# Performance work log

Hardware: AMD Instinct MI355X
Metric: run time of the kernel (lower is better)

## Reference

```python
import jax, jax.numpy as jnp
import numpy as np

NL = 4      # num_hidden_layers
NH = 12     # self-attn heads
CH = 4      # cross-attn heads (hardcoded in module)
S = 4       # speakers per dialog
EPS = 1e-5

def layernorm(x, g, b):
    m = x.mean(-1, keepdims=True)
    v = jnp.mean((x - m) ** 2, axis=-1, keepdims=True)
    return (x - m) * jax.lax.rsqrt(v + EPS) * g + b

def self_mha(x, in_w, in_b, out_w, out_b):
    # x: [B,T,L,H] self-attention over L (the per-turn token axis)
    B, T, L, H = x.shape
    dh = H // NH
    qkv = x @ in_w + in_b                       # [B,T,L,3H]
    q, k, v = jnp.split(qkv, 3, axis=-1)
    q = q.reshape(B, T, L, NH, dh); k = k.reshape(B, T, L, NH, dh); v = v.reshape(B, T, L, NH, dh)
    s = jnp.einsum('btqhd,btkhd->bthqk', q, k) / np.sqrt(dh).astype(x.dtype)
    a = jax.nn.softmax(s, axis=-1)
    o = jnp.einsum('bthqk,btkhd->btqhd', a, v).reshape(B, T, L, H)
    return o @ out_w + out_b

def forward(input_ids, attention_mask, speaker_ids, tok_emb, pos_emb, turn_emb,
            mha_in_w, mha_in_b, mha_out_w, mha_out_b,
            ffn_w1, ffn_b1, ffn_w2, ffn_b2,
            ln1_g, ln1_b, ln2_g, ln2_b,
            gate_w, gate_b, sn_g, sn_b,
            ca_in_w, ca_in_b, ca_out_w, ca_out_b):
    B, T, L = input_ids.shape
    H = tok_emb.shape[1]
    X = tok_emb[input_ids] + pos_emb[jnp.arange(L)][None, None] + turn_emb[jnp.arange(T)][None, :, None]
    mask = attention_mask[..., None].astype(X.dtype)            # [B,T,L,1]
    onehot = (speaker_ids[..., None] == jnp.arange(S)).astype(X.dtype)  # [B,T,S]
    counts = onehot.sum(1)                                      # [B,S]
    M = jnp.zeros((B, S, H), X.dtype)                           # speaker memory
    for l in range(NL):
        m_t = jnp.einsum('bts,bsh->bth', onehot, M)             # gather memory per turn
        h = (X + m_t[:, :, None, :]) * mask                     # mask applied by zeroing inputs (as in source)
        h = self_mha(h, mha_in_w[l], mha_in_b[l], mha_out_w[l], mha_out_b[l])
        h = layernorm(h + X, ln1_g[l], ln1_b[l])
        ffn = jax.nn.gelu(h @ ffn_w1[l] + ffn_b1[l], approximate=False) @ ffn_w2[l] + ffn_b2[l]
        h = layernorm(h + ffn, ln2_g[l], ln2_b[l])
        X = h
        tc = h.mean(2)                                          # token_context [B,T,H]
        # cross-attention: each turn's context queries its dialog's speaker memory
        wq, wk, wv = jnp.split(ca_in_w[l], 3, axis=-1)
        bq, bk, bv = jnp.split(ca_in_b[l], 3)
        dh = H // CH
        q = (tc @ wq + bq).reshape(B, T, CH, dh)
        k = (M @ wk + bk).reshape(B, S, CH, dh)
        v = (M @ wv + bv).reshape(B, S, CH, dh)
        s = jnp.einsum('bthd,bshd->bhts', q, k) / np.sqrt(dh).astype(X.dtype)
        a = jax.nn.softmax(s, axis=-1)
        cc = jnp.einsum('bhts,bshd->bthd', a, v).reshape(B, T, H) @ ca_out_w[l] + ca_out_b[l]
        fused = jnp.concatenate([tc, m_t, cc], axis=-1)         # [B,T,3H]
        upd = layernorm(fused @ gate_w[l] + gate_b[l] + m_t, sn_g[l], sn_b[l])
        # scatter: per-speaker mean over that speaker's turns; untouched speakers keep old memory
        sums = jnp.einsum('bts,bth->bsh', onehot, upd)
        mean = sums / jnp.maximum(counts, 1.0)[..., None]
        M = jnp.where((counts > 0)[..., None], mean, M)
    return X, M

def setup_inputs() -> dict:
    key = jax.random.key(0)
    ks = iter(jax.random.split(key, 32))
    B, T, L, H, F, V, P = 8, 64, 64, 768, 3072, 30522, 512
    n = lambda shape: jax.random.normal(next(ks), shape, jnp.float32) * 0.02
    return {
        'input_ids': jax.random.randint(next(ks), (B, T, L), 0, V, jnp.int32),
        'attention_mask': jax.random.randint(next(ks), (B, T, L), 0, 2, jnp.int32),
        'speaker_ids': jax.random.randint(next(ks), (B, T), 0, S, jnp.int32),
        'tok_emb': n((V, H)), 'pos_emb': n((P, H)), 'turn_emb': n((P, H)),
        'mha_in_w': n((NL, H, 3 * H)), 'mha_in_b': jnp.zeros((NL, 3 * H)),
        'mha_out_w': n((NL, H, H)), 'mha_out_b': jnp.zeros((NL, H)),
        'ffn_w1': n((NL, H, F)), 'ffn_b1': jnp.zeros((NL, F)),
        'ffn_w2': n((NL, F, H)), 'ffn_b2': jnp.zeros((NL, H)),
        'ln1_g': jnp.ones((NL, H)), 'ln1_b': jnp.zeros((NL, H)),
        'ln2_g': jnp.ones((NL, H)), 'ln2_b': jnp.zeros((NL, H)),
        'gate_w': n((NL, 3 * H, H)), 'gate_b': jnp.zeros((NL, H)),
        'sn_g': jnp.ones((NL, H)), 'sn_b': jnp.zeros((NL, H)),
        'ca_in_w': n((NL, H, 3 * H)), 'ca_in_b': jnp.zeros((NL, 3 * H)),
        'ca_out_w': n((NL, H, H)), 'ca_out_b': jnp.zeros((NL, H)),
    }

def reference(input_ids, attention_mask, speaker_ids, tok_emb, pos_emb, turn_emb,
              mha_in_w, mha_in_b, mha_out_w, mha_out_b,
              ffn_w1, ffn_b1, ffn_w2, ffn_b2,
              ln1_g, ln1_b, ln2_g, ln2_b,
              gate_w, gate_b, sn_g, sn_b,
              ca_in_w, ca_in_b, ca_out_w, ca_out_b):
    return forward(input_ids, attention_mask, speaker_ids, tok_emb, pos_emb, turn_emb,
                   mha_in_w, mha_in_b, mha_out_w, mha_out_b,
                   ffn_w1, ffn_b1, ffn_w2, ffn_b2,
                   ln1_g, ln1_b, ln2_g, ln2_b,
                   gate_w, gate_b, sn_g, sn_b,
                   ca_in_w, ca_in_b, ca_out_w, ca_out_b)
```

## Files before the change

### kernel.cpp

```cpp
#include <hip/hip_runtime.h>

using u16 = unsigned short;
using u32 = unsigned int;

#define DI __device__ __forceinline__

typedef __bf16 bf16x8 __attribute__((ext_vector_type(8)));
typedef float  f32x4  __attribute__((ext_vector_type(4)));

DI float b2f(u16 u){ u32 x = ((u32)u) << 16; float f; __builtin_memcpy(&f, &x, 4); return f; }
DI u16 f2b(float f){ __bf16 h = (__bf16)f; u16 r; __builtin_memcpy(&r, &h, 2); return r; }
DI float gelu_fast(float v){
    float u = v * (0.7978845608f + 0.0356774081f * v * v);
    float e = __expf(2.0f * u);
    float t = 1.0f - 2.0f / (e + 1.0f);
    return 0.5f * v * (1.0f + t);
}

#define GLOAD16(g, l) __builtin_amdgcn_global_load_lds( \
    (const __attribute__((address_space(1))) void*)(g), \
    (__attribute__((address_space(3))) void*)(l), 16, 0, 0)

DI bf16x8 ldsr128(const u16* p) {
    bf16x8 r;
    asm volatile("ds_read_b128 %0, %1"
                 : "=v"(r)
                 : "v"((const __attribute__((address_space(3))) u16*)p));
    return r;
}

template<int EPI>
__global__ __launch_bounds__(512, 1)
void gemm256p(const u16* __restrict__ A, const u16* __restrict__ Bt,
              const float* __restrict__ bias, void* __restrict__ Cout,
              int M, int N, int K)
{
    __shared__ u16 lA[2][256 * 64];
    __shared__ u16 lB[2][256 * 64];
    const int tid  = threadIdx.x;
    const int lane = tid & 63;
    const int w    = tid >> 6;
    const int wm   = w >> 2, wn = w & 3;

    const int nx = gridDim.x;
    const int nb = nx * gridDim.y;
    int bid = blockIdx.y * nx + blockIdx.x;
    if ((nb & 7) == 0) bid = ((bid & 7) * (nb >> 3)) + (bid >> 3);
    const int m0 = (bid / nx) * 256;
    const int n0 = (bid % nx) * 256;

    f32x4 acc[8][4] = {};

    const int srowb = w * 32 + (lane >> 3);
    const int csrc  = ((lane & 7) ^ ((lane >> 3) & 7)) * 8;
    const u16* gA[4];
    const u16* gB[4];
    #pragma unroll
    for (int i = 0; i < 4; ++i) {
        int ra = m0 + srowb + i * 8; if (ra > M - 1) ra = M - 1;
        gA[i] = A  + (size_t)ra * K + csrc;
        gB[i] = Bt + (size_t)(n0 + srowb + i * 8) * K + csrc;
    }

    const int la = lane & 15, lg = lane >> 4;
    const int nt = K >> 6;

    #pragma unroll
    for (int i = 0; i < 4; ++i) GLOAD16(gA[i], &lA[0][(w * 256 + i * 64 + lane) * 8]);
    #pragma unroll
    for (int i = 0; i < 4; ++i) GLOAD16(gB[i], &lB[0][(w * 256 + i * 64 + lane) * 8]);
    asm volatile("s_waitcnt vmcnt(0)" ::: "memory");
    __builtin_amdgcn_s_barrier();
    asm volatile("" ::: "memory");

    for (int t = 0; t < nt; ++t) {
        const int p = t & 1;
        const u16* lAp = lA[p];
        const u16* lBp = lB[p];
        u16* dA = lA[p ^ 1];
        u16* dB = lB[p ^ 1];
        const int kn = (t + 1) << 6;
        const bool more = (t + 1 < nt);

        bf16x8 bf[4][2];

        #pragma unroll
        for (int ph = 0; ph < 4; ++ph) {
            if (ph == 0) {
                #pragma unroll
                for (int j = 0; j < 4; ++j) {
                    bf[j][0] = ldsr128(&lBp[(wn * 64 + j * 16 + la) * 64 + (((0 * 4 + lg) ^ (la & 7)) * 8)]);
                    bf[j][1] = ldsr128(&lBp[(wn * 64 + j * 16 + la) * 64 + (((1 * 4 + lg) ^ (la & 7)) * 8)]);
                }
            }
            bf16x8 a0k0 = ldsr128(&lAp[(wm * 128 + (2 * ph) * 16 + la) * 64     + (((0 * 4 + lg) ^ (la & 7)) * 8)]);
            bf16x8 a0k1 = ldsr128(&lAp[(wm * 128 + (2 * ph) * 16 + la) * 64     + (((1 * 4 + lg) ^ (la & 7)) * 8)]);
            bf16x8 a1k0 = ldsr128(&lAp[(wm * 128 + (2 * ph + 1) * 16 + la) * 64 + (((0 * 4 + lg) ^ (la & 7)) * 8)]);
            bf16x8 a1k1 = ldsr128(&lAp[(wm * 128 + (2 * ph + 1) * 16 + la) * 64 + (((1 * 4 + lg) ^ (la & 7)) * 8)]);

            if (ph == 0 && more) {
                #pragma unroll
                for (int i = 0; i < 4; ++i) GLOAD16(gA[i] + kn, &dA[(w * 256 + i * 64 + lane) * 8]);
            }
            if (ph == 1 && more) {
                #pragma unroll
                for (int i = 0; i < 4; ++i) GLOAD16(gB[i] + kn, &dB[(w * 256 + i * 64 + lane) * 8]);
            }

            __builtin_amdgcn_s_barrier();
            asm volatile("s_waitcnt lgkmcnt(0)" ::: "memory");
            __builtin_amdgcn_sched_barrier(0);

            __builtin_amdgcn_s_setprio(1);
            #pragma unroll
            for (int j = 0; j < 4; ++j) {
                acc[2 * ph][j]     = __builtin_amdgcn_mfma_f32_16x16x32_bf16(a0k0, bf[j][0], acc[2 * ph][j],     0, 0, 0);
                acc[2 * ph + 1][j] = __builtin_amdgcn_mfma_f32_16x16x32_bf16(a1k0, bf[j][0], acc[2 * ph + 1][j], 0, 0, 0);
            }
            #pragma unroll
            for (int j = 0; j < 4; ++j) {
                acc[2 * ph][j]     = __builtin_amdgcn_mfma_f32_16x16x32_bf16(a0k1, bf[j][1], acc[2 * ph][j],     0, 0, 0);
                acc[2 * ph + 1][j] = __builtin_amdgcn_mfma_f32_16x16x32_bf16(a1k1, bf[j][1], acc[2 * ph + 1][j], 0, 0, 0);
            }
            __builtin_amdgcn_s_setprio(0);

            if (ph == 3) {
                asm volatile("s_waitcnt vmcnt(0)" ::: "memory");
            }
            __builtin_amdgcn_s_barrier();
            asm volatile("" ::: "memory");
        }
    }

    #pragma unroll
    for (int i = 0; i < 8; i++) {
        const int rowb = m0 + wm * 128 + i * 16 + lg * 4;
        #pragma unroll
        for (int j = 0; j < 4; j++) {
            const int col = n0 + wn * 64 + j * 16 + la;
            const float bv = bias[col];
            #pragma unroll
            for (int r = 0; r < 4; r++) {
                const int rr = rowb + r;
                if (rr < M) {
                    float v = acc[i][j][r] + bv;
                    if constexpr (EPI == 1) v = gelu_fast(v);
                    if constexpr (EPI == 2) ((float*)Cout)[(size_t)rr * N + col] = v;
                    else                    ((u16*)Cout)[(size_t)rr * N + col] = f2b(v);
                }
            }
        }
    }
}

template<int EPI>
__global__ __launch_bounds__(256)
void gemm_bt(const u16* __restrict__ A, const u16* __restrict__ Bt,
             const float* __restrict__ bias, void* __restrict__ Cout,
             int M, int N, int K)
{
    __shared__ u16 lA[3][128 * 32];
    __shared__ u16 lB[3][128 * 32];
    const int tid  = threadIdx.x;
    const int lane = tid & 63;
    const int w    = tid >> 6;
    const int wm   = w >> 1, wn = w & 1;

    const int nx = gridDim.x;
    const int nb = nx * gridDim.y;
    int bid = blockIdx.y * nx + blockIdx.x;
    if ((nb & 7) == 0) bid = ((bid & 7) * (nb >> 3)) + (bid >> 3);
    const int m0 = (bid / nx) * 128;
    const int n0 = (bid % nx) * 128;

    f32x4 acc[4][4] = {};

    const int srow = tid >> 2;
    const int scol = (((tid & 3) ^ ((tid >> 3) & 3)) * 8);
    int ar0 = m0 + srow;      if (ar0 > M - 1) ar0 = M - 1;
    int ar1 = m0 + 64 + srow; if (ar1 > M - 1) ar1 = M - 1;
    const u16* gA0 = A  + (size_t)ar0 * K + scol;
    const u16* gA1 = A  + (size_t)ar1 * K + scol;
    const u16* gB0 = Bt + (size_t)(n0 + srow) * K + scol;
    const u16* gB1 = Bt + (size_t)(n0 + 64 + srow) * K + scol;

    const int la = lane & 15, lg = lane >> 4;
    const int cp = (lg ^ ((la >> 1) & 3)) * 8;

    const int nt = K >> 5;

    GLOAD16(gA0,      &lA[0][tid * 8]);
    GLOAD16(gA1,      &lA[0][tid * 8 + 2048]);
    GLOAD16(gB0,      &lB[0][tid * 8]);
    GLOAD16(gB1,      &lB[0][tid * 8 + 2048]);
    GLOAD16(gA0 + 32, &lA[1][tid * 8]);
    GLOAD16(gA1 + 32, &lA[1][tid * 8 + 2048]);
    GLOAD16(gB0 + 32, &lB[1][tid * 8]);
    GLOAD16(gB1 + 32, &lB[1][tid * 8 + 2048]);

    int cur = 0, pre = 2;
    for (int t = 0; t < nt; ++t) {
        if (t + 1 < nt) asm volatile("s_waitcnt vmcnt(4)" ::: "memory");
        else            asm volatile("s_waitcnt vmcnt(0)" ::: "memory");
        __builtin_amdgcn_s_barrier();
        asm volatile("" ::: "memory");

        if (t + 2 < nt) {
            const int k0 = (t + 2) << 5;
            GLOAD16(gA0 + k0, &lA[pre][tid * 8]);
            GLOAD16(gA1 + k0, &lA[pre][tid * 8 + 2048]);
            GLOAD16(gB0 + k0, &lB[pre][tid * 8]);
            GLOAD16(gB1 + k0, &lB[pre][tid * 8 + 2048]);
        }

        bf16x8 af[4], bfr[4];
        #pragma unroll
        for (int i = 0; i < 4; i++)
            af[i] = ldsr128(&lA[cur][(wm * 64 + i * 16 + la) * 32 + cp]);
        #pragma unroll
        for (int j = 0; j < 4; j++)
            bfr[j] = ldsr128(&lB[cur][(wn * 64 + j * 16 + la) * 32 + cp]);
        asm volatile("s_waitcnt lgkmcnt(0)" ::: "memory");
        __builtin_amdgcn_sched_barrier(0);

        #pragma unroll
        for (int i = 0; i < 4; i++)
            #pragma unroll
            for (int j = 0; j < 4; j++)
                acc[i][j] = __builtin_amdgcn_mfma_f32_16x16x32_bf16(af[i], bfr[j], acc[i][j], 0, 0, 0);

        cur = (cur == 2) ? 0 : cur + 1;
        pre = (pre == 2) ? 0 : pre + 1;
    }

    #pragma unroll
    for (int i = 0; i < 4; i++) {
        const int rowb = m0 + wm * 64 + i * 16 + lg * 4;
        #pragma unroll
        for (int j = 0; j < 4; j++) {
            const int col = n0 + wn * 64 + j * 16 + la;
            const float bv = bias[col];
            #pragma unroll
            for (int r = 0; r < 4; r++) {
                const int rr = rowb + r;
                if (rr < M) {
                    float v = acc[i][j][r] + bv;
                    if constexpr (EPI == 1) v = gelu_fast(v);
                    if constexpr (EPI == 2) ((float*)Cout)[(size_t)rr * N + col] = v;
                    else                    ((u16*)Cout)[(size_t)rr * N + col] = f2b(v);
                }
            }
        }
    }
}

__global__ __launch_bounds__(256)
void transp_conv(const float* __restrict__ in, u16* __restrict__ out, int K, int N)
{
    __shared__ float tile[32][33];
    const int l = blockIdx.z;
    const float* inp = in + (size_t)l * K * N;
    u16* op = out + (size_t)l * K * N;
    const int kb = blockIdx.y * 32, nb = blockIdx.x * 32;
    const int tx = threadIdx.x, ty = threadIdx.y;
    #pragma unroll
    for (int i = 0; i < 32; i += 8)
        tile[ty + i][tx] = inp[(size_t)(kb + ty + i) * N + nb + tx];
    __syncthreads();
    #pragma unroll
    for (int i = 0; i < 32; i += 8)
        op[(size_t)(nb + ty + i) * K + kb + tx] = f2b(tile[tx][ty + i]);
}

__global__ __launch_bounds__(192)
void embed_k(const int* __restrict__ ids, const float* __restrict__ te,
             const float* __restrict__ pe, const float* __restrict__ ue,
             u16* __restrict__ X)
{
    const int tok = blockIdx.x;
    const int l = tok & 63;
    const int t = (tok >> 6) & 63;
    const int id = ids[tok];
    const int c = threadIdx.x * 4;
    float4 a = *(const float4*)&te[(size_t)id * 768 + c];
    float4 p = *(const float4*)&pe[(size_t)l * 768 + c];
    float4 u = *(const float4*)&ue[(size_t)t * 768 + c];
    ushort4 o;
    o.x = f2b(a.x + p.x + u.x); o.y = f2b(a.y + p.y + u.y);
    o.z = f2b(a.z + p.z + u.z); o.w = f2b(a.w + p.w + u.w);
    *(ushort4*)&X[(size_t)tok * 768 + c] = o;
}

__global__ __launch_bounds__(192)
void gather_mt(const float* __restrict__ M, const int* __restrict__ sid,
               float* __restrict__ mt)
{
    const int bt = blockIdx.x, b = bt >> 6, tid = threadIdx.x;
    const float* src = M + ((size_t)b * 4 + sid[bt]) * 768;
    *(float4*)&mt[(size_t)bt * 768 + tid * 4] = *(const float4*)&src[tid * 4];
}

__global__ __launch_bounds__(192)
void prep_ain(const u16* __restrict__ X, const float* __restrict__ mt,
              const int* __restrict__ mask, u16* __restrict__ Ain)
{
    const int tok = blockIdx.x, bt = tok >> 6;
    const float mk = (float)mask[tok];
    const int c = threadIdx.x * 4;
    ushort4 xv = *(const ushort4*)&X[(size_t)tok * 768 + c];
    float4 mv = *(const float4*)&mt[(size_t)bt * 768 + c];
    ushort4 o;
    o.x = f2b((b2f(xv.x) + mv.x) * mk); o.y = f2b((b2f(xv.y) + mv.y) * mk);
    o.z = f2b((b2f(xv.z) + mv.z) * mk); o.w = f2b((b2f(xv.w) + mv.w) * mk);
    *(ushort4*)&Ain[(size_t)tok * 768 + c] = o;
}

DI int swz(int row, int col) { return row * 64 + (((col >> 3) ^ (row & 7)) << 3) + (col & 7); }

__global__ __launch_bounds__(256)
void attn_self(const u16* __restrict__ QKV, u16* __restrict__ O)
{
    __shared__ u16 lQ[64 * 64], lK[64 * 64], lVt[64 * 64], lP[64 * 64];
    __shared__ float lS[64 * 68];
    const int bt = blockIdx.x / 12, h = blockIdx.x % 12;
    const int tid = threadIdx.x, lane = tid & 63, w = tid >> 6;
    const size_t base = (size_t)bt * 64 * 2304;

    #pragma unroll
    for (int it = 0; it < 2; ++it) {
        const int slot = it * 256 + tid;
        const int l = slot >> 3, dc = (slot & 7) * 8;
        const u16* qp = QKV + base + (size_t)l * 2304 + h * 64 + dc;
        *(uint4*)&lQ[swz(l, dc)] = *(const uint4*)qp;
        *(uint4*)&lK[swz(l, dc)] = *(const uint4*)(qp + 768);
        uint4 vv = *(const uint4*)(qp + 1536);
        u16 tmp[8]; *(uint4*)tmp = vv;
        #pragma unroll
        for (int j = 0; j < 8; j++) lVt[swz(dc + j, l)] = tmp[j];
    }
    __syncthreads();

    const int la = lane & 15, lg = lane >> 4;
    {
        f32x4 sa[4] = {};
        #pragma unroll
        for (int kh = 0; kh < 64; kh += 32) {
            bf16x8 aq = *(const bf16x8*)&lQ[swz(w * 16 + la, kh + lg * 8)];
            #pragma unroll
            for (int fn = 0; fn < 4; ++fn) {
                bf16x8 bk = *(const bf16x8*)&lK[swz(fn * 16 + la, kh + lg * 8)];
                sa[fn] = __builtin_amdgcn_mfma_f32_16x16x32_bf16(aq, bk, sa[fn], 0, 0, 0);
            }
        }
        #pragma unroll
        for (int fn = 0; fn < 4; ++fn)
            #pragma unroll
            for (int r = 0; r < 4; ++r)
                lS[(w * 16 + lg * 4 + r) * 68 + fn * 16 + la] = sa[fn][r] * 0.125f;
    }
    __syncthreads();

    {
        const int row = tid >> 2, q4 = tid & 3;
        float e[16]; float mx = -1e30f;
        #pragma unroll
        for (int j = 0; j < 16; j++) { e[j] = lS[row * 68 + q4 * 16 + j]; mx = fmaxf(mx, e[j]); }
        mx = fmaxf(mx, __shfl_xor(mx, 1)); mx = fmaxf(mx, __shfl_xor(mx, 2));
        float sm = 0.f;
        #pragma unroll
        for (int j = 0; j < 16; j++) { e[j] = __expf(e[j] - mx); sm += e[j]; }
        sm += __shfl_xor(sm, 1); sm += __shfl_xor(sm, 2);
        const float inv = 1.0f / sm;
        #pragma unroll
        for (int j = 0; j < 16; j++) lP[swz(row, q4 * 16 + j)] = f2b(e[j] * inv);
    }
    __syncthreads();

    {
        f32x4 oa[4] = {};
        #pragma unroll
        for (int kh = 0; kh < 64; kh += 32) {
            bf16x8 ap = *(const bf16x8*)&lP[swz(w * 16 + la, kh + lg * 8)];
            #pragma unroll
            for (int fn = 0; fn < 4; ++fn) {
                bf16x8 bv = *(const bf16x8*)&lVt[swz(fn * 16 + la, kh + lg * 8)];
                oa[fn] = __builtin_amdgcn_mfma_f32_16x16x32_bf16(ap, bv, oa[fn], 0, 0, 0);
            }
        }
        const size_t ob = (size_t)bt * 64 * 768 + h * 64;
        #pragma unroll
        for (int fn = 0; fn < 4; ++fn)
            #pragma unroll
            for (int r = 0; r < 4; ++r)
                O[ob + (size_t)(w * 16 + lg * 4 + r) * 768 + fn * 16 + la] = f2b(oa[fn][r]);
    }
}

DI float wave_red(float v) {
    #pragma unroll
    for (int o = 32; o > 0; o >>= 1) v += __shfl_xor(v, o);
    return v;
}

__global__ __launch_bounds__(192)
void ln_res(const u16* __restrict__ a, const u16* __restrict__ b,
            const float* __restrict__ g, const float* __restrict__ be,
            u16* __restrict__ out)
{
    __shared__ float red[6];
    const int tid = threadIdx.x, w = tid >> 6;
    const size_t off = (size_t)blockIdx.x * 768 + tid * 4;
    ushort4 av = *(const ushort4*)&a[off];
    ushort4 bv = *(const ushort4*)&b[off];
    float x0 = b2f(av.x) + b2f(bv.x);
    float x1 = b2f(av.y) + b2f(bv.y);
    float x2 = b2f(av.z) + b2f(bv.z);
    float x3 = b2f(av.w) + b2f(bv.w);
    float s  = wave_red(x0 + x1 + x2 + x3);
    float ss = wave_red(x0 * x0 + x1 * x1 + x2 * x2 + x3 * x3);
    if ((tid & 63) == 0) { red[w] = s; red[3 + w] = ss; }
    __syncthreads();
    s = red[0] + red[1] + red[2];
    ss = red[3] + red[4] + red[5];
    const float mean = s * (1.f / 768.f);
    const float var = fmaxf(ss * (1.f / 768.f) - mean * mean, 0.f);
    const float inv = rsqrtf(var + 1e-5f);
    const int c = tid * 4;
    float4 gv = *(const float4*)&g[c];
    float4 ev = *(const float4*)&be[c];
    ushort4 o;
    o.x = f2b((x0 - mean) * inv * gv.x + ev.x);
    o.y = f2b((x1 - mean) * inv * gv.y + ev.y);
    o.z = f2b((x2 - mean) * inv * gv.z + ev.z);
    o.w = f2b((x3 - mean) * inv * gv.w + ev.w);
    *(ushort4*)&out[off] = o;
}

__global__ __launch_bounds__(192)
void ln_upd(const float* __restrict__ a, const float* __restrict__ b,
            const float* __restrict__ g, const float* __restrict__ be,
            float* __restrict__ out)
{
    __shared__ float red[6];
    const int tid = threadIdx.x, w = tid >> 6;
    const size_t off = (size_t)blockIdx.x * 768 + tid * 4;
    float4 av = *(const float4*)&a[off];
    float4 bv = *(const float4*)&b[off];
    float x0 = av.x + bv.x, x1 = av.y + bv.y, x2 = av.z + bv.z, x3 = av.w + bv.w;
    float s  = wave_red(x0 + x1 + x2 + x3);
    float ss = wave_red(x0 * x0 + x1 * x1 + x2 * x2 + x3 * x3);
    if ((tid & 63) == 0) { red[w] = s; red[3 + w] = ss; }
    __syncthreads();
    s = red[0] + red[1] + red[2];
    ss = red[3] + red[4] + red[5];
    const float mean = s * (1.f / 768.f);
    const float var = fmaxf(ss * (1.f / 768.f) - mean * mean, 0.f);
    const float inv = rsqrtf(var + 1e-5f);
    const int c = tid * 4;
    float4 gv = *(const float4*)&g[c];
    float4 ev = *(const float4*)&be[c];
    float4 o;
    o.x = (x0 - mean) * inv * gv.x + ev.x;
    o.y = (x1 - mean) * inv * gv.y + ev.y;
    o.z = (x2 - mean) * inv * gv.z + ev.z;
    o.w = (x3 - mean) * inv * gv.w + ev.w;
    *(float4*)&out[off] = o;
}

__global__ __launch_bounds__(192)
void tc_mean(const u16* __restrict__ X, u16* __restrict__ tcb)
{
    const int bt = blockIdx.x, tid = threadIdx.x;
    const u16* base = X + (size_t)bt * 64 * 768 + tid * 4;
    float s0 = 0, s1 = 0, s2 = 0, s3 = 0;
    for (int l = 0; l < 64; ++l) {
        ushort4 v = *(const ushort4*)&base[(size_t)l * 768];
        s0 += b2f(v.x); s1 += b2f(v.y); s2 += b2f(v.z); s3 += b2f(v.w);
    }
    ushort4 o;
    o.x = f2b(s0 * (1.f / 64.f)); o.y = f2b(s1 * (1.f / 64.f));
    o.z = f2b(s2 * (1.f / 64.f)); o.w = f2b(s3 * (1.f / 64.f));
    *(ushort4*)&tcb[(size_t)bt * 768 + tid * 4] = o;
}

__global__ __launch_bounds__(256)
void conv_bf16(const float* __restrict__ in, u16* __restrict__ out, int n)
{
    const int i = blockIdx.x * 256 + threadIdx.x;
    if (i < n) out[i] = f2b(in[i]);
}

__global__ __launch_bounds__(256)
void zero_f32(float* __restrict__ buf, int n)
{
    const int i = blockIdx.x * 256 + threadIdx.x;
    if (i < n) buf[i] = 0.f;
}

__global__ __launch_bounds__(256)
void cross_attn(const u16* __restrict__ qc, const u16* __restrict__ kvc,
                u16* __restrict__ cca)
{
    __shared__ float q[768], kk[4][768], vv[4][768], sraw[16], aw[16];
    const int bt = blockIdx.x, b = bt >> 6, tid = threadIdx.x;
    #pragma unroll
    for (int i = 0; i < 3; i++) q[tid + i * 256] = b2f(qc[(size_t)bt * 768 + tid + i * 256]);
    #pragma unroll
    for (int i = 0; i < 12; i++) {
        const int idx = i * 256 + tid;
        const int s = idx / 768, d = idx % 768;
        kk[s][d] = b2f(kvc[(size_t)(b * 4 + s) * 1536 + d]);
        vv[s][d] = b2f(kvc[(size_t)(b * 4 + s) * 1536 + 768 + d]);
    }
    __syncthreads();
    if (tid < 16) {
        const int hh = tid >> 2, s = tid & 3;
        float acc = 0.f;
        for (int d = 0; d < 192; ++d) acc += q[hh * 192 + d] * kk[s][hh * 192 + d];
        sraw[tid] = acc * 0.07216878364870323f;
    }
    __syncthreads();
    if (tid < 4) {
        float m = -1e30f;
        for (int s = 0; s < 4; s++) m = fmaxf(m, sraw[tid * 4 + s]);
        float ee[4], sm = 0.f;
        for (int s = 0; s < 4; s++) { ee[s] = __expf(sraw[tid * 4 + s] - m); sm += ee[s]; }
        for (int s = 0; s < 4; s++) aw[tid * 4 + s] = ee[s] / sm;
    }
    __syncthreads();
    #pragma unroll
    for (int i = 0; i < 3; i++) {
        const int j = tid + i * 256;
        const int hh = j / 192;
        float v = aw[hh * 4 + 0] * vv[0][j] + aw[hh * 4 + 1] * vv[1][j]
                + aw[hh * 4 + 2] * vv[2][j] + aw[hh * 4 + 3] * vv[3][j];
        cca[(size_t)bt * 768 + j] = f2b(v);
    }
}

__global__ __launch_bounds__(256)
void concat_fused(const u16* __restrict__ tcb, const float* __restrict__ mt,
                  const u16* __restrict__ ccp, u16* __restrict__ Fu)
{
    const int bt = blockIdx.x, tid = threadIdx.x;
    u16* o = Fu + (size_t)bt * 2304;
    #pragma unroll
    for (int i = 0; i < 3; i++) {
        const int j = tid + i * 256;
        o[j]        = tcb[(size_t)bt * 768 + j];
        o[768 + j]  = f2b(mt[(size_t)bt * 768 + j]);
        o[1536 + j] = ccp[(size_t)bt * 768 + j];
    }
}

__global__ __launch_bounds__(256)
void scatter_mem(const float* __restrict__ upd, const int* __restrict__ sid,
                 const float* __restrict__ counts, float* __restrict__ M)
{
    const int bs = blockIdx.x, b = bs >> 2, s = bs & 3, tid = threadIdx.x;
    const float c = counts[bs];
    #pragma unroll
    for (int i = 0; i < 3; i++) {
        const int j = tid + i * 256;
        float acc = 0.f;
        for (int t = 0; t < 64; ++t)
            if (sid[b * 64 + t] == s) acc += upd[((size_t)b * 64 + t) * 768 + j];
        if (c > 0.f) M[(size_t)bs * 768 + j] = acc / fmaxf(c, 1.f);
    }
}

__global__ void calc_counts(const int* __restrict__ sid, float* __restrict__ counts)
{
    const int tid = threadIdx.x;
    if (tid < 32) {
        const int b = tid >> 2, s = tid & 3;
        float c = 0.f;
        for (int t = 0; t < 64; ++t) c += (sid[b * 64 + t] == s) ? 1.f : 0.f;
        counts[tid] = c;
    }
}

__global__ __launch_bounds__(256)
void final_out(const u16* __restrict__ Xb, const float* __restrict__ M,
               float* __restrict__ out)
{
    const size_t i4 = ((size_t)blockIdx.x * 256 + threadIdx.x) * 4;
    const size_t NX = 25165824ull;
    if (i4 < NX) {
        ushort4 v = *(const ushort4*)&Xb[i4];
        float4 o; o.x = b2f(v.x); o.y = b2f(v.y); o.z = b2f(v.z); o.w = b2f(v.w);
        *(float4*)&out[i4] = o;
    } else if (i4 < NX + 24576ull) {
        *(float4*)&out[i4] = *(const float4*)&M[i4 - NX];
    }
}

extern "C" void kernel_launch(void* const* d_in, const int* in_sizes, int n_in,
                              void* d_out, int out_size, void* d_ws, size_t ws_size,
                              hipStream_t stream)
{
    const int*   input_ids = (const int*)d_in[0];
    const int*   attn_mask = (const int*)d_in[1];
    const int*   sid       = (const int*)d_in[2];
    const float* tok_emb   = (const float*)d_in[3];
    const float* pos_emb   = (const float*)d_in[4];
    const float* turn_emb  = (const float*)d_in[5];
    const float* mha_in_w  = (const float*)d_in[6];
    const float* mha_in_b  = (const float*)d_in[7];
    const float* mha_out_w = (const float*)d_in[8];
    const float* mha_out_b = (const float*)d_in[9];
    const float* ffn_w1    = (const float*)d_in[10];
    const float* ffn_b1    = (const float*)d_in[11];
    const float* ffn_w2    = (const float*)d_in[12];
    const float* ffn_b2    = (const float*)d_in[13];
    const float* ln1_g     = (const float*)d_in[14];
    const float* ln1_b     = (const float*)d_in[15];
    const float* ln2_g     = (const float*)d_in[16];
    const float* ln2_b     = (const float*)d_in[17];
    const float* gate_w    = (const float*)d_in[18];
    const float* gate_b    = (const float*)d_in[19];
    const float* sn_g      = (const float*)d_in[20];
    const float* sn_b      = (const float*)d_in[21];
    const float* ca_in_w   = (const float*)d_in[22];
    const float* ca_in_b   = (const float*)d_in[23];
    const float* ca_out_w  = (const float*)d_in[24];
    const float* ca_out_b  = (const float*)d_in[25];
    (void)in_sizes; (void)n_in; (void)out_size;

    const size_t MB = 1ull << 20;
    int NCA, NCF; bool allW;
    if      (ws_size >= 460 * MB) { NCA = 2; NCF = 1; allW = true;  }
    else if (ws_size >= 340 * MB) { NCA = 2; NCF = 2; allW = true;  }
    else if (ws_size >= 255 * MB) { NCA = 2; NCF = 2; allW = false; }
    else                          { NCA = 4; NCF = 4; allW = false; }
    const int MRA = 32768 / NCA;
    const int MRF = 32768 / NCF;
    const size_t wl = allW ? 4 : 1;

    char* p = (char*)d_ws;
    auto alloc = [&](size_t n) { void* r = p; p += (n + 255) & ~(size_t)255; return r; };
    u16*   Xb    = (u16*)alloc(50331648);
    u16*   Hb    = (u16*)alloc(50331648);
    u16*   WqkvT = (u16*)alloc(wl * 3538944);
    u16*   WoT   = (u16*)alloc(wl * 1179648);
    u16*   W1T   = (u16*)alloc(wl * 4718592);
    u16*   W2T   = (u16*)alloc(wl * 4718592);
    u16*   WgT   = (u16*)alloc(wl * 3538944);
    u16*   WcaT  = (u16*)alloc(wl * 3538944);
    u16*   WcoT  = (u16*)alloc(wl * 1179648);
    float* mt    = (float*)alloc(1572864);
    u16*   tcb   = (u16*)alloc(786432);
    u16*   Mb    = (u16*)alloc(49152);
    u16*   qc    = (u16*)alloc(786432);
    u16*   kvc   = (u16*)alloc(98304);
    u16*   cca   = (u16*)alloc(786432);
    u16*   ccp   = (u16*)alloc(786432);
    u16*   Fu    = (u16*)alloc(2359296);
    float* gout  = (float*)alloc(1572864);
    float* upd   = (float*)alloc(1572864);
    float* cnts  = (float*)alloc(256);
    float* M     = (float*)alloc(98304);

    u16 *A, *QKVb, *Gb;
    if (NCF == 1) {
        A    = (u16*)alloc(50331648);
        Gb   = (u16*)alloc(201326592);
        QKVb = (u16*)d_out;
    } else if (NCF == 2) {
        A    = (u16*)alloc(50331648);
        QKVb = (u16*)alloc((size_t)MRA * 2304 * 2);
        Gb   = (u16*)d_out;
    } else {
        Gb   = (u16*)alloc((size_t)MRF * 3072 * 2);
        A    = (u16*)d_out;
        QKVb = (u16*)d_out + 25165824;
    }
    u16* Obuf = Gb;

    zero_f32<<<96, 256, 0, stream>>>(M, 24576);
    calc_counts<<<1, 64, 0, stream>>>(sid, cnts);
    embed_k<<<32768, 192, 0, stream>>>(input_ids, tok_emb, pos_emb, turn_emb, Xb);

    if (allW) {
        transp_conv<<<dim3(72, 24, 4), dim3(32, 8), 0, stream>>>(mha_in_w,  WqkvT, 768, 2304);
        transp_conv<<<dim3(24, 24, 4), dim3(32, 8), 0, stream>>>(mha_out_w, WoT,   768, 768);
        transp_conv<<<dim3(96, 24, 4), dim3(32, 8), 0, stream>>>(ffn_w1,    W1T,   768, 3072);
        transp_conv<<<dim3(24, 96, 4), dim3(32, 8), 0, stream>>>(ffn_w2,    W2T,  3072, 768);
        transp_conv<<<dim3(24, 72, 4), dim3(32, 8), 0, stream>>>(gate_w,    WgT,  2304, 768);
        transp_conv<<<dim3(72, 24, 4), dim3(32, 8), 0, stream>>>(ca_in_w,   WcaT,  768, 2304);
        transp_conv<<<dim3(24, 24, 4), dim3(32, 8), 0, stream>>>(ca_out_w,  WcoT,  768, 768);
    }

    for (int l = 0; l < 4; ++l) {
        if (!allW) {
            transp_conv<<<dim3(72, 24), dim3(32, 8), 0, stream>>>(mha_in_w  + (size_t)l * 768 * 2304, WqkvT, 768, 2304);
            transp_conv<<<dim3(24, 24), dim3(32, 8), 0, stream>>>(mha_out_w + (size_t)l * 768 * 768,  WoT,   768, 768);
            transp_conv<<<dim3(96, 24), dim3(32, 8), 0, stream>>>(ffn_w1    + (size_t)l * 768 * 3072, W1T,   768, 3072);
            transp_conv<<<dim3(24, 96), dim3(32, 8), 0, stream>>>(ffn_w2    + (size_t)l * 3072 * 768, W2T,  3072, 768);
            transp_conv<<<dim3(24, 72), dim3(32, 8), 0, stream>>>(gate_w    + (size_t)l * 2304 * 768, WgT,  2304, 768);
            transp_conv<<<dim3(72, 24), dim3(32, 8), 0, stream>>>(ca_in_w   + (size_t)l * 768 * 2304, WcaT,  768, 2304);
            transp_conv<<<dim3(24, 24), dim3(32, 8), 0, stream>>>(ca_out_w  + (size_t)l * 768 * 768,  WcoT,  768, 768);
        }
        const u16* Wqkv_l = WqkvT + (size_t)(allW ? l : 0) * 2304 * 768;
        const u16* Wo_l   = WoT   + (size_t)(allW ? l : 0) * 768 * 768;
        const u16* W1_l   = W1T   + (size_t)(allW ? l : 0) * 768 * 3072;
        const u16* W2_l   = W2T   + (size_t)(allW ? l : 0) * 3072 * 768;
        const u16* Wg_l   = WgT   + (size_t)(allW ? l : 0) * 2304 * 768;
        const u16* Wca_l  = WcaT  + (size_t)(allW ? l : 0) * 768 * 2304;
        const u16* Wco_l  = WcoT  + (size_t)(allW ? l : 0) * 768 * 768;

        gather_mt<<<512, 192, 0, stream>>>(M, sid, mt);
        prep_ain<<<32768, 192, 0, stream>>>(Xb, mt, attn_mask, A);

        for (int c = 0; c < NCA; ++c) {
            u16* Ac = A + (size_t)c * MRA * 768;
            gemm256p<0><<<dim3(9, MRA / 256), 512, 0, stream>>>(Ac, Wqkv_l, mha_in_b + l * 2304, QKVb, MRA, 2304, 768);
            attn_self<<<(MRA / 64) * 12, 256, 0, stream>>>(QKVb, Obuf);
            gemm_bt<0><<<dim3(6, MRA / 128), 256, 0, stream>>>(Obuf, Wo_l, mha_out_b + l * 768, Ac, MRA, 768, 768);
        }
        ln_res<<<32768, 192, 0, stream>>>(A, Xb, ln1_g + l * 768, ln1_b + l * 768, Hb);

        for (int c = 0; c < NCF; ++c) {
            u16* Hc = Hb + (size_t)c * MRF * 768;
            u16* Ac = A  + (size_t)c * MRF * 768;
            gemm256p<1><<<dim3(12, MRF / 256), 512, 0, stream>>>(Hc, W1_l, ffn_b1 + l * 3072, Gb, MRF, 3072, 768);
            gemm_bt<0><<<dim3(6, MRF / 128), 256, 0, stream>>>(Gb, W2_l, ffn_b2 + l * 768, Ac, MRF, 768, 3072);
        }
        ln_res<<<32768, 192, 0, stream>>>(A, Hb, ln2_g + l * 768, ln2_b + l * 768, Xb);

        tc_mean<<<512, 192, 0, stream>>>(Xb, tcb);
        conv_bf16<<<96, 256, 0, stream>>>(M, Mb, 24576);
        gemm_bt<0><<<dim3(6, 4), 256, 0, stream>>>(tcb, Wca_l, ca_in_b + l * 2304, qc, 512, 768, 768);
        gemm_bt<0><<<dim3(12, 1), 256, 0, stream>>>(Mb, Wca_l + 768 * 768, ca_in_b + l * 2304 + 768, kvc, 32, 1536, 768);
        cross_attn<<<512, 256, 0, stream>>>(qc, kvc, cca);
        gemm_bt<0><<<dim3(6, 4), 256, 0, stream>>>(cca, Wco_l, ca_out_b + l * 768, ccp, 512, 768, 768);
        concat_fused<<<512, 256, 0, stream>>>(tcb, mt, ccp, Fu);
        gemm_bt<2><<<dim3(6, 4), 256, 0, stream>>>(Fu, Wg_l, gate_b + l * 768, gout, 512, 768, 2304);
        ln_upd<<<512, 192, 0, stream>>>(gout, mt, sn_g + l * 768, sn_b + l * 768, upd);
        scatter_mem<<<32, 256, 0, stream>>>(upd, sid, cnts, M);
    }

    final_out<<<24600, 256, 0, stream>>>(Xb, M, (float*)d_out);
}
```

Before: 4.186 ms.

## Switch 256x256 GEMM to triple-buffered K=32 pipeline with two-stage prefetch

The 256x256 MFMA GEMM used for the QKV and FFN-up projections now uses three LDS stages of K=32 in place of two stages of K=64. Global-to-LDS loads run two tiles ahead, with a new swizzle and load mapping for the narrower tile. This aims to hide global memory latency better while keeping the LDS footprint about the same. In exchange it halves the MFMA work per barrier and adds more barriers and waitcnt bookkeeping per K step.

```diff
diff --git a/kernel.cpp b/kernel.cpp
--- a/kernel.cpp
+++ b/kernel.cpp
@@ -31,12 +31,12 @@
 
 template<int EPI>
 __global__ __launch_bounds__(512, 1)
-void gemm256p(const u16* __restrict__ A, const u16* __restrict__ Bt,
+void gemm256c(const u16* __restrict__ A, const u16* __restrict__ Bt,
               const float* __restrict__ bias, void* __restrict__ Cout,
               int M, int N, int K)
 {
-    __shared__ u16 lA[2][256 * 64];
-    __shared__ u16 lB[2][256 * 64];
+    __shared__ u16 lA[3][256 * 32];
+    __shared__ u16 lB[3][256 * 32];
     const int tid  = threadIdx.x;
     const int lane = tid & 63;
     const int w    = tid >> 6;
@@ -51,85 +51,94 @@
 
     f32x4 acc[8][4] = {};
 
-    const int srowb = w * 32 + (lane >> 3);
-    const int csrc  = ((lane & 7) ^ ((lane >> 3) & 7)) * 8;
-    const u16* gA[4];
-    const u16* gB[4];
-    #pragma unroll
-    for (int i = 0; i < 4; ++i) {
-        int ra = m0 + srowb + i * 8; if (ra > M - 1) ra = M - 1;
-        gA[i] = A  + (size_t)ra * K + csrc;
-        gB[i] = Bt + (size_t)(n0 + srowb + i * 8) * K + csrc;
-    }
+    const int srow = tid >> 2;
+    const int scol = (((tid & 3) ^ ((tid >> 3) & 3)) * 8);
+    int ar0 = m0 + srow;       if (ar0 > M - 1) ar0 = M - 1;
+    int ar1 = m0 + 128 + srow; if (ar1 > M - 1) ar1 = M - 1;
+    const u16* gA0 = A  + (size_t)ar0 * K + scol;
+    const u16* gA1 = A  + (size_t)ar1 * K + scol;
+    const u16* gB0 = Bt + (size_t)(n0 + srow) * K + scol;
+    const u16* gB1 = Bt + (size_t)(n0 + 128 + srow) * K + scol;
 
     const int la = lane & 15, lg = lane >> 4;
-    const int nt = K >> 6;
-
-    #pragma unroll
-    for (int i = 0; i < 4; ++i) GLOAD16(gA[i], &lA[0][(w * 256 + i * 64 + lane) * 8]);
-    #pragma unroll
-    for (int i = 0; i < 4; ++i) GLOAD16(gB[i], &lB[0][(w * 256 + i * 64 + lane) * 8]);
-    asm volatile("s_waitcnt vmcnt(0)" ::: "memory");
+    const int cp = (lg ^ ((la >> 1) & 3)) * 8;
+
+    const int nt = K >> 5;
+
+    GLOAD16(gA0,      &lA[0][tid * 8]);
+    GLOAD16(gA1,      &lA[0][4096 + tid * 8]);
+    GLOAD16(gB0,      &lB[0][tid * 8]);
+    GLOAD16(gB1,      &lB[0][4096 + tid * 8]);
+    GLOAD16(gA0 + 32, &lA[1][tid * 8]);
+    GLOAD16(gA1 + 32, &lA[1][4096 + tid * 8]);
+    GLOAD16(gB0 + 32, &lB[1][tid * 8]);
+    GLOAD16(gB1 + 32, &lB[1][4096 + tid * 8]);
+
+    asm volatile("s_waitcnt vmcnt(4)" ::: "memory");
     __builtin_amdgcn_s_barrier();
     asm volatile("" ::: "memory");
 
+    int cur = 0;
     for (int t = 0; t < nt; ++t) {
-        const int p = t & 1;
-        const u16* lAp = lA[p];
-        const u16* lBp = lB[p];
-        u16* dA = lA[p ^ 1];
-        u16* dB = lB[p ^ 1];
-        const int kn = (t + 1) << 6;
-        const bool more = (t + 1 < nt);
-
-        bf16x8 bf[4][2];
-
-        #pragma unroll
-        for (int ph = 0; ph < 4; ++ph) {
-            if (ph == 0) {
-                #pragma unroll
-                for (int j = 0; j < 4; ++j) {
-                    bf[j][0] = ldsr128(&lBp[(wn * 64 + j * 16 + la) * 64 + (((0 * 4 + lg) ^ (la & 7)) * 8)]);
-                    bf[j][1] = ldsr128(&lBp[(wn * 64 + j * 16 + la) * 64 + (((1 * 4 + lg) ^ (la & 7)) * 8)]);
-                }
-            }
-            bf16x8 a0k0 = ldsr128(&lAp[(wm * 128 + (2 * ph) * 16 + la) * 64     + (((0 * 4 + lg) ^ (la & 7)) * 8)]);
-            bf16x8 a0k1 = ldsr128(&lAp[(wm * 128 + (2 * ph) * 16 + la) * 64     + (((1 * 4 + lg) ^ (la & 7)) * 8)]);
-            bf16x8 a1k0 = ldsr128(&lAp[(wm * 128 + (2 * ph + 1) * 16 + la) * 64 + (((0 * 4 + lg) ^ (la & 7)) * 8)]);
-            bf16x8 a1k1 = ldsr128(&lAp[(wm * 128 + (2 * ph + 1) * 16 + la) * 64 + (((1 * 4 + lg) ^ (la & 7)) * 8)]);
-
-            if (ph == 0 && more) {
-                #pragma unroll
-                for (int i = 0; i < 4; ++i) GLOAD16(gA[i] + kn, &dA[(w * 256 + i * 64 + lane) * 8]);
-            }
-            if (ph == 1 && more) {
-                #pragma unroll
-                for (int i = 0; i < 4; ++i) GLOAD16(gB[i] + kn, &dB[(w * 256 + i * 64 + lane) * 8]);
-            }
-
-            __builtin_amdgcn_s_barrier();
-            asm volatile("s_waitcnt lgkmcnt(0)" ::: "memory");
-            __builtin_amdgcn_sched_barrier(0);
-
-            __builtin_amdgcn_s_setprio(1);
-            #pragma unroll
-            for (int j = 0; j < 4; ++j) {
-                acc[2 * ph][j]     = __builtin_amdgcn_mfma_f32_16x16x32_bf16(a0k0, bf[j][0], acc[2 * ph][j],     0, 0, 0);
-                acc[2 * ph + 1][j] = __builtin_amdgcn_mfma_f32_16x16x32_bf16(a1k0, bf[j][0], acc[2 * ph + 1][j], 0, 0, 0);
-            }
-            #pragma unroll
-            for (int j = 0; j < 4; ++j) {
-                acc[2 * ph][j]     = __builtin_amdgcn_mfma_f32_16x16x32_bf16(a0k1, bf[j][1], acc[2 * ph][j],     0, 0, 0);
-                acc[2 * ph + 1][j] = __builtin_amdgcn_mfma_f32_16x16x32_bf16(a1k1, bf[j][1], acc[2 * ph + 1][j], 0, 0, 0);
-            }
-            __builtin_amdgcn_s_setprio(0);
-
-            if (ph == 3) {
-                asm volatile("s_waitcnt vmcnt(0)" ::: "memory");
-            }
-            __builtin_amdgcn_s_barrier();
-            asm volatile("" ::: "memory");
-        }
+        const u16* lAp = lA[cur];
+        const u16* lBp = lB[cur];
+        const int nxt = (cur >= 1) ? cur - 1 : cur + 2;
+        const int k2 = (t + 2) << 5;
+        const bool more = (t + 2 < nt);
+
+        bf16x8 bfr[4], af[4];
+
+        #pragma unroll
+        for (int j = 0; j < 4; ++j)
+            bfr[j] = ldsr128(&lBp[(wn * 64 + j * 16 + la) * 32 + cp]);
+        #pragma unroll
+        for (int i = 0; i < 4; ++i)
+            af[i] = ldsr128(&lAp[(wm * 128 + i * 16 + la) * 32 + cp]);
+        if (more) {
+            GLOAD16(gA0 + k2, &lA[nxt][tid * 8]);
+            GLOAD16(gA1 + k2, &lA[nxt][4096 + tid * 8]);
+        }
+        __builtin_amdgcn_s_barrier();
+        asm volatile("s_waitcnt lgkmcnt(0)" ::: "memory");
+        __builtin_amdgcn_sched_barrier(0);
+
+        __builtin_amdgcn_s_setprio(1);
+        #pragma unroll
+        for (int i = 0; i < 4; ++i)
+            #pragma unroll
+            for (int j = 0; j < 4; ++j)
+                acc[i][j] = __builtin_amdgcn_mfma_f32_16x16x32_bf16(af[i], bfr[j], acc[i][j], 0, 0, 0);
+        __builtin_amdgcn_s_setprio(0);
+        __builtin_amdgcn_s_barrier();
+        asm volatile("" ::: "memory");
+
+        #pragma unroll
+        for (int i = 0; i < 4; ++i)
+            af[i] = ldsr128(&lAp[(wm * 128 + (i + 4) * 16 + la) * 32 + cp]);
+        if (more) {
+            GLOAD16(gB0 + k2, &lB[nxt][tid * 8]);
+            GLOAD16(gB1 + k2, &lB[nxt][4096 + tid * 8]);
+        }
+        __builtin_amdgcn_s_barrier();
+        asm volatile("s_waitcnt lgkmcnt(0)" ::: "memory");
+        __builtin_amdgcn_sched_barrier(0);
+
+        __builtin_amdgcn_s_setprio(1);
+        #pragma unroll
+        for (int i = 0; i < 4; ++i)
+            #pragma unroll
+            for (int j = 0; j < 4; ++j)
+                acc[i + 4][j] = __builtin_amdgcn_mfma_f32_16x16x32_bf16(af[i], bfr[j], acc[i + 4][j], 0, 0, 0);
+        __builtin_amdgcn_s_setprio(0);
+
+        if (t + 1 < nt) {
+            if (more) asm volatile("s_waitcnt vmcnt(4)" ::: "memory");
+            else      asm volatile("s_waitcnt vmcnt(0)" ::: "memory");
+        }
+        __builtin_amdgcn_s_barrier();
+        asm volatile("" ::: "memory");
+
+        cur = (cur + 1 == 3) ? 0 : cur + 1;
     }
 
     #pragma unroll
@@ -714,7 +723,7 @@
 
         for (int c = 0; c < NCA; ++c) {
             u16* Ac = A + (size_t)c * MRA * 768;
-            gemm256p<0><<<dim3(9, MRA / 256), 512, 0, stream>>>(Ac, Wqkv_l, mha_in_b + l * 2304, QKVb, MRA, 2304, 768);
+            gemm256c<0><<<dim3(9, MRA / 256), 512, 0, stream>>>(Ac, Wqkv_l, mha_in_b + l * 2304, QKVb, MRA, 2304, 768);
             attn_self<<<(MRA / 64) * 12, 256, 0, stream>>>(QKVb, Obuf);
             gemm_bt<0><<<dim3(6, MRA / 128), 256, 0, stream>>>(Obuf, Wo_l, mha_out_b + l * 768, Ac, MRA, 768, 768);
         }
@@ -723,7 +732,7 @@
         for (int c = 0; c < NCF; ++c) {
             u16* Hc = Hb + (size_t)c * MRF * 768;
             u16* Ac = A  + (size_t)c * MRF * 768;
-            gemm256p<1><<<dim3(12, MRF / 256), 512, 0, stream>>>(Hc, W1_l, ffn_b1 + l * 3072, Gb, MRF, 3072, 768);
+            gemm256c<1><<<dim3(12, MRF / 256), 512, 0, stream>>>(Hc, W1_l, ffn_b1 + l * 3072, Gb, MRF, 3072, 768);
             gemm_bt<0><<<dim3(6, MRF / 128), 256, 0, stream>>>(Gb, W2_l, ffn_b2 + l * 768, Ac, MRF, 768, 3072);
         }
         ln_res<<<32768, 192, 0, stream>>>(A, Hb, ln2_g + l * 768, ln2_b + l * 768, Xb);
```

Result: no change. 4.187 ms (+0.0%).
